# Kernel optimization log

Hardware: AMD Instinct MI355X
Metric: run time of the kernel (lower is better)

The kernel has to match this reference:

```python
import jax, jax.numpy as jnp
import numpy as np

H, W, C = 2048, 2048, 8
N = 4_194_304


def setup_inputs() -> dict:
    key = jax.random.key(0)
    k1, k2 = jax.random.split(key, 2)
    coords = jax.random.uniform(k1, (N, 2), jnp.float32, 0.0, float(H - 1))
    visible = jax.random.normal(k2, (H, W, C), jnp.float32)
    bias = jnp.zeros((2,), jnp.float32)
    return {"coords": coords, "visible": visible, "bias": bias}


def _interp(idx, visible):
    # Faithful translation of linear_interpolation forward.
    hw = jnp.asarray(visible.shape[:-1], jnp.float32)  # [H, W]
    c = jnp.maximum(idx, 0.0)
    low = jnp.minimum(jnp.floor(c), hw - 2.0)
    delta = c - low                                     # [N, 2]
    i = low.astype(jnp.int32)
    i0, i1 = i[:, 0], i[:, 1]
    tl = visible[i0,     i1]       # idx_low
    tr = visible[i0 + 1, i1]       # idx_low + [1, 0]
    bl = visible[i0,     i1 + 1]   # idx_low + [0, 1]
    br = visible[i0 + 1, i1 + 1]   # idx_low + [1, 1]
    d0 = delta[:, :1]   # delta along first axis, broadcast over channels
    d1 = delta[:, 1:2]  # delta along second axis
    mid_bottom = br + d0 * (bl - br)
    mid_top    = tr + d0 * (tl - tr)
    interp = mid_bottom + d1 * (mid_top - mid_bottom)   # [N, C]
    return interp


def reference(coords, visible, bias):
    idx = coords.astype(jnp.float32) - bias
    return _interp(idx, visible)
```

## Files before the change

### kernel.cpp

```cpp
#include <hip/hip_runtime.h>

#define IMG_H 2048
#define IMG_W 2048
#define IMG_C 8

#define KBINS      64
#define SLAB_SHIFT 5
#define SPT        16
#define SBLOCK     256

__device__ __forceinline__ float4 lerp4(float4 tl, float4 tr, float4 bl, float4 br,
                                        float d0, float d1) {
    float4 o;
    float mb, mt;
    mb = br.x + d0 * (bl.x - br.x); mt = tr.x + d0 * (tl.x - tr.x); o.x = mb + d1 * (mt - mb);
    mb = br.y + d0 * (bl.y - br.y); mt = tr.y + d0 * (tl.y - tr.y); o.y = mb + d1 * (mt - mb);
    mb = br.z + d0 * (bl.z - br.z); mt = tr.z + d0 * (tl.z - tr.z); o.z = mb + d1 * (mt - mb);
    mb = br.w + d0 * (bl.w - br.w); mt = tr.w + d0 * (tl.w - tr.w); o.w = mb + d1 * (mt - mb);
    return o;
}

__global__ __launch_bounds__(SBLOCK) void scatter_kernel(
    const float* __restrict__ coords,
    const float* __restrict__ visible,
    const float* __restrict__ bias,
    float* __restrict__ out,
    unsigned* __restrict__ cursor,
    unsigned* __restrict__ recIdx,
    float* __restrict__ recX,
    float* __restrict__ recY,
    int n, unsigned cap)
{
    __shared__ unsigned hist[KBINS];
    __shared__ unsigned basev[KBINS];
    __shared__ unsigned lofs[KBINS];

    int t = threadIdx.x;
    if (t < KBINS) hist[t] = 0;
    __syncthreads();

    int blockStart = blockIdx.x * (SBLOCK * SPT);
    float b0 = bias[0];
    float b1 = bias[1];

    for (int k = 0; k < SPT; ++k) {
        int s = blockStart + k * SBLOCK + t;
        if (s < n) {
            float cx = coords[2 * (size_t)s];
            float c0 = fmaxf(cx - b0, 0.0f);
            float low0 = fminf(floorf(c0), (float)(IMG_H - 2));
            int i0 = (int)low0;
            atomicAdd(&hist[i0 >> SLAB_SHIFT], 1u);
        }
    }
    __syncthreads();

    if (t < KBINS) {
        basev[t] = atomicAdd(&cursor[t], hist[t]);
        lofs[t] = 0;
    }
    __syncthreads();

    for (int k = 0; k < SPT; ++k) {
        int s = blockStart + k * SBLOCK + t;
        if (s < n) {
            float2 cv = *(const float2*)(coords + 2 * (size_t)s);
            float c0 = fmaxf(cv.x - b0, 0.0f);
            float low0 = fminf(floorf(c0), (float)(IMG_H - 2));
            int i0 = (int)low0;
            int b = i0 >> SLAB_SHIFT;
            unsigned off = atomicAdd(&lofs[b], 1u);
            unsigned slot = basev[b] + off;
            if (slot < cap) {
                size_t g = (size_t)b * cap + slot;
                recIdx[g] = (unsigned)s;
                recX[g] = cv.x;
                recY[g] = cv.y;
            } else {
                float c1 = fmaxf(cv.y - b1, 0.0f);
                float low1 = fminf(floorf(c1), (float)(IMG_W - 2));
                float d0 = c0 - low0;
                float d1 = c1 - low1;
                int i1 = (int)low1;
                const float* pt = visible + ((size_t)i0 * IMG_W + (size_t)i1) * IMG_C;
                const float* pb = pt + (size_t)IMG_W * IMG_C;
                for (int q = 0; q < 2; ++q) {
                    float4 tl = *(const float4*)(pt + 4 * q);
                    float4 bl = *(const float4*)(pt + 8 + 4 * q);
                    float4 tr = *(const float4*)(pb + 4 * q);
                    float4 br = *(const float4*)(pb + 8 + 4 * q);
                    float4 o = lerp4(tl, tr, bl, br, d0, d1);
                    *(float4*)(out + (size_t)s * IMG_C + 4 * q) = o;
                }
            }
        }
    }
}

__global__ __launch_bounds__(256) void gather_kernel(
    const float* __restrict__ visible,
    const float* __restrict__ bias,
    const unsigned* __restrict__ cursor,
    const unsigned* __restrict__ recIdx,
    const float* __restrict__ recX,
    const float* __restrict__ recY,
    float* __restrict__ out,
    unsigned cap, unsigned long long magicM)
{
    unsigned tid = blockIdx.x * blockDim.x + threadIdx.x;
    unsigned j = tid >> 1;
    unsigned part = tid & 1;
    if (j >= (unsigned)KBINS * cap) return;

    unsigned b = (unsigned)(((unsigned long long)j * magicM) >> 40);
    unsigned pos = j - b * cap;
    unsigned cnt = cursor[b];
    cnt = cnt > cap ? cap : cnt;
    if (pos >= cnt) return;

    unsigned s = recIdx[j];
    float cx = recX[j];
    float cy = recY[j];
    float b0 = bias[0];
    float b1 = bias[1];

    float c0 = fmaxf(cx - b0, 0.0f);
    float c1 = fmaxf(cy - b1, 0.0f);
    float low0 = fminf(floorf(c0), (float)(IMG_H - 2));
    float low1 = fminf(floorf(c1), (float)(IMG_W - 2));
    float d0 = c0 - low0;
    float d1 = c1 - low1;
    int i0 = (int)low0;
    int i1 = (int)low1;

    const float* p_t = visible + ((size_t)i0 * IMG_W + (size_t)i1) * IMG_C + part * 4;
    const float* p_b = p_t + (size_t)IMG_W * IMG_C;

    float4 tl = *(const float4*)(p_t);
    float4 bl = *(const float4*)(p_t + 8);
    float4 tr = *(const float4*)(p_b);
    float4 br = *(const float4*)(p_b + 8);

    float4 o = lerp4(tl, tr, bl, br, d0, d1);

    *(float4*)(out + (size_t)s * IMG_C + part * 4) = o;
}

__global__ __launch_bounds__(256) void idx2pixel_simple(
    const float* __restrict__ coords,
    const float* __restrict__ visible,
    const float* __restrict__ bias,
    float* __restrict__ out,
    int n)
{
    int tid = blockIdx.x * blockDim.x + threadIdx.x;
    int s = tid >> 1;
    int part = tid & 1;
    if (s >= n) return;

    float2 cv = *(const float2*)(coords + 2 * (size_t)s);
    float b0 = bias[0];
    float b1 = bias[1];

    float c0 = fmaxf(cv.x - b0, 0.0f);
    float c1 = fmaxf(cv.y - b1, 0.0f);
    float low0 = fminf(floorf(c0), (float)(IMG_H - 2));
    float low1 = fminf(floorf(c1), (float)(IMG_W - 2));
    float d0 = c0 - low0;
    float d1 = c1 - low1;
    int i0 = (int)low0;
    int i1 = (int)low1;

    const float* p_t = visible + ((size_t)i0 * IMG_W + (size_t)i1) * IMG_C + part * 4;
    const float* p_b = p_t + (size_t)IMG_W * IMG_C;

    float4 tl = *(const float4*)(p_t);
    float4 bl = *(const float4*)(p_t + 8);
    float4 tr = *(const float4*)(p_b);
    float4 br = *(const float4*)(p_b + 8);

    float4 o = lerp4(tl, tr, bl, br, d0, d1);
    *(float4*)(out + (size_t)s * IMG_C + part * 4) = o;
}

extern "C" void kernel_launch(void* const* d_in, const int* in_sizes, int n_in,
                              void* d_out, int out_size, void* d_ws, size_t ws_size,
                              hipStream_t stream) {
    const float* coords  = (const float*)d_in[0];
    const float* visible = (const float*)d_in[1];
    const float* bias    = (const float*)d_in[2];
    float* out = (float*)d_out;

    int n = in_sizes[0] / 2;
    if (n <= 0) return;

    unsigned cap = (unsigned)((unsigned long long)n / KBINS * 106ull / 100ull + 1024ull);
    size_t need = 256 + (size_t)KBINS * cap * 12;

    if (ws_size < need) {
        long long threads = 2LL * n;
        int block = 256;
        long long grid = (threads + block - 1) / block;
        idx2pixel_simple<<<(int)grid, block, 0, stream>>>(coords, visible, bias, out, n);
        return;
    }

    unsigned* cursor = (unsigned*)d_ws;
    unsigned* recIdx = (unsigned*)((char*)d_ws + 256);
    float* recX = (float*)(recIdx + (size_t)KBINS * cap);
    float* recY = recX + (size_t)KBINS * cap;

    hipMemsetAsync(cursor, 0, KBINS * sizeof(unsigned), stream);

    int sblocks = (n + SBLOCK * SPT - 1) / (SBLOCK * SPT);
    scatter_kernel<<<sblocks, SBLOCK, 0, stream>>>(
        coords, visible, bias, out, cursor, recIdx, recX, recY, n, cap);

    unsigned long long magicM = ((1ull << 40) + cap - 1) / cap;
    long long threads = 2LL * KBINS * (long long)cap;
    int gblocks = (int)((threads + 255) / 256);
    gather_kernel<<<gblocks, 256, 0, stream>>>(
        visible, bias, cursor, recIdx, recX, recY, out, cap, magicM);
}
```

Before: 472.4 us.

## Bin points into 2D 32x32 tiles and gather from an LDS-staged tile

Replaces the 64 row-slab bins with 4096 two-dimensional 32x32 pixel tiles. The gather kernel now uses one block per tile: it stages the 33x33x8 image patch in shared memory and interpolates every point in that bin from LDS rather than through scattered global reads. The scatter kernel uses larger blocks with more samples each and a 4096-entry shared histogram, and capacity is now sized from the available workspace. In exchange, shared-memory use per block grows, global atomic traffic to cursors rises, and per-bin workload is uneven.

```diff
diff --git a/kernel.cpp b/kernel.cpp
--- a/kernel.cpp
+++ b/kernel.cpp
@@ -1,13 +1,20 @@
 #include <hip/hip_runtime.h>
 
-#define IMG_H 2048
-#define IMG_W 2048
-#define IMG_C 8
-
-#define KBINS      64
-#define SLAB_SHIFT 5
-#define SPT        16
-#define SBLOCK     256
+#define IMG_H  2048
+#define IMG_W  2048
+#define IMG_C  8
+#define IMG_WF (IMG_W * IMG_C)
+
+#define TILE   32
+#define TB     (IMG_H / TILE)
+#define KBINS  (TB * TB)
+#define TLR    (TILE + 1)
+#define TLC    ((TILE + 1) * IMG_C)
+#define TLF4   (TLR * (TLC / 4))
+
+#define SBLOCK 512
+#define SPT    32
+#define GBLOCK 256
 
 __device__ __forceinline__ float4 lerp4(float4 tl, float4 tr, float4 bl, float4 br,
                                         float d0, float d1) {
@@ -18,6 +25,14 @@
     mb = br.z + d0 * (bl.z - br.z); mt = tr.z + d0 * (tl.z - tr.z); o.z = mb + d1 * (mt - mb);
     mb = br.w + d0 * (bl.w - br.w); mt = tr.w + d0 * (tl.w - tr.w); o.w = mb + d1 * (mt - mb);
     return o;
+}
+
+__device__ __forceinline__ int bin2d(float cx, float cy, float b0, float b1) {
+    float c0 = fmaxf(cx - b0, 0.0f);
+    float c1 = fmaxf(cy - b1, 0.0f);
+    float low0 = fminf(floorf(c0), (float)(IMG_H - 2));
+    float low1 = fminf(floorf(c1), (float)(IMG_W - 2));
+    return ((int)low0 >> 5) * TB + ((int)low1 >> 5);
 }
 
 __global__ __launch_bounds__(SBLOCK) void scatter_kernel(
@@ -36,39 +51,34 @@
     __shared__ unsigned lofs[KBINS];
 
     int t = threadIdx.x;
-    if (t < KBINS) hist[t] = 0;
-    __syncthreads();
-
-    int blockStart = blockIdx.x * (SBLOCK * SPT);
+    for (int u = t; u < KBINS; u += SBLOCK) hist[u] = 0;
+    __syncthreads();
+
+    long long blockStart = (long long)blockIdx.x * (SBLOCK * SPT);
     float b0 = bias[0];
     float b1 = bias[1];
 
     for (int k = 0; k < SPT; ++k) {
-        int s = blockStart + k * SBLOCK + t;
-        if (s < n) {
-            float cx = coords[2 * (size_t)s];
-            float c0 = fmaxf(cx - b0, 0.0f);
-            float low0 = fminf(floorf(c0), (float)(IMG_H - 2));
-            int i0 = (int)low0;
-            atomicAdd(&hist[i0 >> SLAB_SHIFT], 1u);
-        }
-    }
-    __syncthreads();
-
-    if (t < KBINS) {
-        basev[t] = atomicAdd(&cursor[t], hist[t]);
-        lofs[t] = 0;
-    }
-    __syncthreads();
-
-    for (int k = 0; k < SPT; ++k) {
-        int s = blockStart + k * SBLOCK + t;
+        long long s = blockStart + (long long)k * SBLOCK + t;
         if (s < n) {
             float2 cv = *(const float2*)(coords + 2 * (size_t)s);
-            float c0 = fmaxf(cv.x - b0, 0.0f);
-            float low0 = fminf(floorf(c0), (float)(IMG_H - 2));
-            int i0 = (int)low0;
-            int b = i0 >> SLAB_SHIFT;
+            atomicAdd(&hist[bin2d(cv.x, cv.y, b0, b1)], 1u);
+        }
+    }
+    __syncthreads();
+
+    for (int u = t; u < KBINS; u += SBLOCK) {
+        unsigned h = hist[u];
+        basev[u] = h ? atomicAdd(&cursor[u], h) : 0u;
+        lofs[u] = 0;
+    }
+    __syncthreads();
+
+    for (int k = 0; k < SPT; ++k) {
+        long long s = blockStart + (long long)k * SBLOCK + t;
+        if (s < n) {
+            float2 cv = *(const float2*)(coords + 2 * (size_t)s);
+            int b = bin2d(cv.x, cv.y, b0, b1);
             unsigned off = atomicAdd(&lofs[b], 1u);
             unsigned slot = basev[b] + off;
             if (slot < cap) {
@@ -77,10 +87,13 @@
                 recX[g] = cv.x;
                 recY[g] = cv.y;
             } else {
+                float c0 = fmaxf(cv.x - b0, 0.0f);
                 float c1 = fmaxf(cv.y - b1, 0.0f);
+                float low0 = fminf(floorf(c0), (float)(IMG_H - 2));
                 float low1 = fminf(floorf(c1), (float)(IMG_W - 2));
                 float d0 = c0 - low0;
                 float d1 = c1 - low1;
+                int i0 = (int)low0;
                 int i1 = (int)low1;
                 const float* pt = visible + ((size_t)i0 * IMG_W + (size_t)i1) * IMG_C;
                 const float* pb = pt + (size_t)IMG_W * IMG_C;
@@ -97,53 +110,75 @@
     }
 }
 
-__global__ __launch_bounds__(256) void gather_kernel(
+__global__ __launch_bounds__(GBLOCK) void gather_tile_kernel(
+    const float* __restrict__ bias,
     const float* __restrict__ visible,
-    const float* __restrict__ bias,
     const unsigned* __restrict__ cursor,
     const unsigned* __restrict__ recIdx,
     const float* __restrict__ recX,
     const float* __restrict__ recY,
     float* __restrict__ out,
-    unsigned cap, unsigned long long magicM)
+    unsigned cap)
 {
-    unsigned tid = blockIdx.x * blockDim.x + threadIdx.x;
-    unsigned j = tid >> 1;
-    unsigned part = tid & 1;
-    if (j >= (unsigned)KBINS * cap) return;
-
-    unsigned b = (unsigned)(((unsigned long long)j * magicM) >> 40);
-    unsigned pos = j - b * cap;
-    unsigned cnt = cursor[b];
-    cnt = cnt > cap ? cap : cnt;
-    if (pos >= cnt) return;
-
-    unsigned s = recIdx[j];
-    float cx = recX[j];
-    float cy = recY[j];
+    __shared__ float tile[TLR * TLC];
+
+    int b  = blockIdx.x;
+    int bh = b >> 6;
+    int bw = b & (TB - 1);
+    int r0  = bh * TILE;
+    int c0f = bw * TILE * IMG_C;
+
+    int t = threadIdx.x;
+
+    for (int v = t; v < TLF4; v += GBLOCK) {
+        int trow = v / (TLC / 4);
+        int tc4  = v - trow * (TLC / 4);
+        int gr = r0 + trow;  if (gr > IMG_H - 1) gr = IMG_H - 1;
+        int gf = c0f + tc4 * 4; if (gf > IMG_WF - 4) gf = IMG_WF - 4;
+        *(float4*)(&tile[trow * TLC + tc4 * 4]) =
+            *(const float4*)(visible + (size_t)gr * IMG_WF + gf);
+    }
+    __syncthreads();
+
     float b0 = bias[0];
     float b1 = bias[1];
 
-    float c0 = fmaxf(cx - b0, 0.0f);
-    float c1 = fmaxf(cy - b1, 0.0f);
-    float low0 = fminf(floorf(c0), (float)(IMG_H - 2));
-    float low1 = fminf(floorf(c1), (float)(IMG_W - 2));
-    float d0 = c0 - low0;
-    float d1 = c1 - low1;
-    int i0 = (int)low0;
-    int i1 = (int)low1;
-
-    const float* p_t = visible + ((size_t)i0 * IMG_W + (size_t)i1) * IMG_C + part * 4;
-    const float* p_b = p_t + (size_t)IMG_W * IMG_C;
-
-    float4 tl = *(const float4*)(p_t);
-    float4 bl = *(const float4*)(p_t + 8);
-    float4 tr = *(const float4*)(p_b);
-    float4 br = *(const float4*)(p_b + 8);
-
-    float4 o = lerp4(tl, tr, bl, br, d0, d1);
-
-    *(float4*)(out + (size_t)s * IMG_C + part * 4) = o;
+    unsigned cnt = cursor[b];
+    if (cnt > cap) cnt = cap;
+    size_t base = (size_t)b * cap;
+
+    for (unsigned j = t; j < cnt; j += GBLOCK) {
+        unsigned s = recIdx[base + j];
+        float cx = recX[base + j];
+        float cy = recY[base + j];
+
+        float cc0 = fmaxf(cx - b0, 0.0f);
+        float cc1 = fmaxf(cy - b1, 0.0f);
+        float low0 = fminf(floorf(cc0), (float)(IMG_H - 2));
+        float low1 = fminf(floorf(cc1), (float)(IMG_W - 2));
+        float d0 = cc0 - low0;
+        float d1 = cc1 - low1;
+        int lr  = (int)low0 - r0;
+        int lcf = (int)low1 * IMG_C - c0f;
+
+        const float* q_t = &tile[lr * TLC + lcf];
+        const float* q_b = q_t + TLC;
+
+        float4 tl0 = *(const float4*)(q_t);
+        float4 bl0 = *(const float4*)(q_t + IMG_C);
+        float4 tr0 = *(const float4*)(q_b);
+        float4 br0 = *(const float4*)(q_b + IMG_C);
+        float4 o0 = lerp4(tl0, tr0, bl0, br0, d0, d1);
+
+        float4 tl1 = *(const float4*)(q_t + 4);
+        float4 bl1 = *(const float4*)(q_t + IMG_C + 4);
+        float4 tr1 = *(const float4*)(q_b + 4);
+        float4 br1 = *(const float4*)(q_b + IMG_C + 4);
+        float4 o1 = lerp4(tl1, tr1, bl1, br1, d0, d1);
+
+        *(float4*)(out + (size_t)s * IMG_C)     = o0;
+        *(float4*)(out + (size_t)s * IMG_C + 4) = o1;
+    }
 }
 
 __global__ __launch_bounds__(256) void idx2pixel_simple(
@@ -194,31 +229,31 @@
     int n = in_sizes[0] / 2;
     if (n <= 0) return;
 
-    unsigned cap = (unsigned)((unsigned long long)n / KBINS * 106ull / 100ull + 1024ull);
-    size_t need = 256 + (size_t)KBINS * cap * 12;
-
-    if (ws_size < need) {
+    size_t curBytes = (size_t)KBINS * sizeof(unsigned);
+    unsigned mean = (unsigned)(((unsigned long long)n + KBINS - 1) / KBINS);
+    unsigned want = mean + mean / 32 + 64;
+    size_t capAvail = (ws_size > curBytes)
+                    ? (ws_size - curBytes) / ((size_t)KBINS * 12u) : 0;
+    unsigned cap = capAvail < (size_t)want ? (unsigned)capAvail : want;
+
+    if (cap < mean + 16) {
         long long threads = 2LL * n;
-        int block = 256;
-        long long grid = (threads + block - 1) / block;
-        idx2pixel_simple<<<(int)grid, block, 0, stream>>>(coords, visible, bias, out, n);
+        long long grid = (threads + 255) / 256;
+        idx2pixel_simple<<<(int)grid, 256, 0, stream>>>(coords, visible, bias, out, n);
         return;
     }
 
     unsigned* cursor = (unsigned*)d_ws;
-    unsigned* recIdx = (unsigned*)((char*)d_ws + 256);
+    unsigned* recIdx = (unsigned*)((char*)d_ws + curBytes);
     float* recX = (float*)(recIdx + (size_t)KBINS * cap);
     float* recY = recX + (size_t)KBINS * cap;
 
-    hipMemsetAsync(cursor, 0, KBINS * sizeof(unsigned), stream);
-
-    int sblocks = (n + SBLOCK * SPT - 1) / (SBLOCK * SPT);
+    hipMemsetAsync(cursor, 0, curBytes, stream);
+
+    int sblocks = (int)(((long long)n + SBLOCK * SPT - 1) / (SBLOCK * SPT));
     scatter_kernel<<<sblocks, SBLOCK, 0, stream>>>(
         coords, visible, bias, out, cursor, recIdx, recX, recY, n, cap);
 
-    unsigned long long magicM = ((1ull << 40) + cap - 1) / cap;
-    long long threads = 2LL * KBINS * (long long)cap;
-    int gblocks = (int)((threads + 255) / 256);
-    gather_kernel<<<gblocks, 256, 0, stream>>>(
-        visible, bias, cursor, recIdx, recX, recY, out, cap, magicM);
-}
+    gather_tile_kernel<<<KBINS, GBLOCK, 0, stream>>>(
+        bias, visible, cursor, recIdx, recX, recY, out, cap);
+}
```

Result: slower. 542.9 us (+14.9%).
